# Kernel optimization log

Hardware: AMD Instinct MI355X
Metric: run time of the kernel (lower is better)

## Reference

```python
import jax, jax.numpy as jnp
import numpy as np

NEG_SLOPE = 0.2


def _gcn_conv(x, edge_index, W, b):
    # Standard GCNConv: y = D^-1/2 (A + I) D^-1/2 (x W) + b
    N = x.shape[0]
    loop = jnp.arange(N, dtype=edge_index.dtype)
    src = jnp.concatenate([edge_index[0], loop])  # [E+N]
    dst = jnp.concatenate([edge_index[1], loop])  # [E+N]
    deg = jax.ops.segment_sum(jnp.ones_like(dst, dtype=x.dtype), dst, num_segments=N)
    dinv = jnp.where(deg > 0, jax.lax.rsqrt(deg), 0.0)
    norm = dinv[src] * dinv[dst]                  # [E+N]
    h = x @ W                                     # [N, out] dense GEMM
    msg = h[src] * norm[:, None]                  # irregular gather, [E+N, out]
    agg = jax.ops.segment_sum(msg, dst, num_segments=N)  # irregular scatter
    return agg + b


def setup_inputs() -> dict:
    key = jax.random.key(0)
    ks = jax.random.split(key, 5)
    N, E, d_in, d_hid = 50000, 800000, 256, 512
    s = lambda fan_in, fan_out: np.sqrt(6.0 / (fan_in + fan_out))
    return {
        "x": jax.random.normal(ks[0], (N, d_in), dtype=jnp.float32),
        "edge_index": jax.random.randint(ks[1], (2, E), 0, N, dtype=jnp.int64),
        "W_gcn": jax.random.uniform(ks[2], (d_in, d_hid), jnp.float32, -s(d_in, d_hid), s(d_in, d_hid)),
        "b_gcn": jnp.zeros((d_hid,), jnp.float32),
        "W2": jax.random.uniform(ks[3], (d_hid, d_hid), jnp.float32, -s(d_hid, d_hid), s(d_hid, d_hid)),
        "b2": jnp.zeros((d_hid,), jnp.float32),
        "W_out": jax.random.uniform(ks[4], (d_hid, 1), jnp.float32, -s(d_hid, 1), s(d_hid, 1)),
        "b_out": jnp.zeros((1,), jnp.float32),
    }


def reference(x, edge_index, W_gcn, b_gcn, W2, b2, W_out, b_out):
    h = _gcn_conv(x, edge_index, W_gcn, b_gcn)           # [N, 512]
    h = jax.nn.leaky_relu(h, NEG_SLOPE)
    h = jax.nn.leaky_relu(h @ W2 + b2, NEG_SLOPE)        # [N, 512]
    return h @ W_out + b_out                             # [N, 1]
```

## Files before the change

### kernel.cpp

```cpp
#include <hip/hip_runtime.h>

#define D_IN  256
#define D_HID 512
#define NEG_SLOPE 0.2f
#define SCAN_CHUNK 2048

typedef __attribute__((ext_vector_type(8))) short short8;
typedef __attribute__((ext_vector_type(4))) float floatx4;

__device__ __forceinline__ unsigned short f2bf(float f) {
    unsigned int u = __float_as_uint(f);
    u += 0x7fffu + ((u >> 16) & 1u);
    return (unsigned short)(u >> 16);
}
__device__ __forceinline__ float bf2f(unsigned short u) {
    return __uint_as_float(((unsigned int)u) << 16);
}

__device__ __forceinline__ int eidx(const void* ei, long pos, int is64) {
    return is64 ? (int)((const long long*)ei)[pos] : ((const int*)ei)[pos];
}

__global__ __launch_bounds__(256) void k_init(int* __restrict__ deg, int N,
                                              const unsigned int* __restrict__ ei,
                                              int npairs, int* flag,
                                              const float* __restrict__ W_gcn,
                                              unsigned short* __restrict__ Wgt,
                                              const float* __restrict__ W2,
                                              unsigned short* __restrict__ W2t,
                                              const float* __restrict__ b_out,
                                              float* __restrict__ out) {
    int t = blockIdx.x * blockDim.x + threadIdx.x;
    if (blockIdx.x == 0) {
        __shared__ int nz;
        if (threadIdx.x == 0) nz = 0;
        __syncthreads();
        for (int p = threadIdx.x; p < npairs; p += blockDim.x)
            if (ei[2 * p + 1] != 0) nz = 1;
        __syncthreads();
        if (threadIdx.x == 0) *flag = nz ? 0 : 1;
    }
    if (t < D_IN * D_HID) {
        int n = t / D_IN, k = t - n * D_IN;
        Wgt[t] = f2bf(W_gcn[(long)k * D_HID + n]);
        return;
    }
    int u = t - D_IN * D_HID;
    if (u < D_HID * D_HID) {
        int n = u / D_HID, k = u - n * D_HID;
        W2t[u] = f2bf(W2[(long)k * D_HID + n]);
        return;
    }
    u -= D_HID * D_HID;
    if (u < N) { deg[u] = 0; out[u] = b_out[0]; }
}

__global__ void k_deg_count(const void* __restrict__ ei, const int* __restrict__ flag,
                            int* __restrict__ deg, int E) {
    int e = blockIdx.x * blockDim.x + threadIdx.x;
    if (e < E) atomicAdd(&deg[eidx(ei, (long)E + e, *flag)], 1);
}

__global__ __launch_bounds__(256) void k_scan1(const int* __restrict__ deg,
                                               int* __restrict__ bsum, int N) {
    int base = blockIdx.x * SCAN_CHUNK;
    int hi = min(base + SCAN_CHUNK, N);
    int s = 0;
    for (int i = base + threadIdx.x; i < hi; i += 256) s += deg[i];
#pragma unroll
    for (int off = 32; off > 0; off >>= 1) s += __shfl_down(s, off, 64);
    __shared__ int lds[4];
    if ((threadIdx.x & 63) == 0) lds[threadIdx.x >> 6] = s;
    __syncthreads();
    if (threadIdx.x == 0) bsum[blockIdx.x] = lds[0] + lds[1] + lds[2] + lds[3];
}

__global__ __launch_bounds__(256) void k_scan23(const int* __restrict__ deg,
                                                const int* __restrict__ bsum, int NB,
                                                int* __restrict__ offs,
                                                int* __restrict__ cursor,
                                                float* __restrict__ dinv, int N) {
    __shared__ int lds[256];
    int t = threadIdx.x;
    int bbase = 0;
    for (int i = 0; i < NB; ++i) bbase += (i < blockIdx.x) ? bsum[i] : 0;
    if (blockIdx.x == NB - 1 && t == 0) offs[N] = bbase + bsum[NB - 1];
    int base = blockIdx.x * SCAN_CHUNK;
    int lo = base + t * 8;
    int v[8], s = 0;
#pragma unroll
    for (int j = 0; j < 8; ++j) {
        int i = lo + j;
        v[j] = (i < N) ? deg[i] : 0;
        s += v[j];
    }
    lds[t] = s;
    __syncthreads();
    for (int d = 1; d < 256; d <<= 1) {
        int add = (t >= d) ? lds[t - d] : 0;
        __syncthreads();
        lds[t] += add;
        __syncthreads();
    }
    int run = bbase + ((t > 0) ? lds[t - 1] : 0);
#pragma unroll
    for (int j = 0; j < 8; ++j) {
        int i = lo + j;
        if (i < N) {
            offs[i] = run; cursor[i] = run;
            dinv[i] = rsqrtf(1.0f + (float)v[j]);
            run += v[j];
        }
    }
}

__global__ __launch_bounds__(256) void k_prescale(const float* __restrict__ x,
                                                  const float* __restrict__ dinv,
                                                  unsigned short* __restrict__ xb, int N) {
    long t = (long)blockIdx.x * blockDim.x + threadIdx.x;
    long total = (long)N * D_IN / 4;
    if (t >= total) return;
    int row = (int)(t >> 6);
    float s = dinv[row];
    float4 v = *(const float4*)(x + t * 4);
    ushort4 o;
    o.x = f2bf(v.x * s); o.y = f2bf(v.y * s); o.z = f2bf(v.z * s); o.w = f2bf(v.w * s);
    *(ushort4*)(xb + t * 4) = o;
}

__global__ void k_fill(const void* __restrict__ ei, const int* __restrict__ flag,
                       int* __restrict__ cursor, int* __restrict__ esrc, int E) {
    int e = blockIdx.x * blockDim.x + threadIdx.x;
    if (e >= E) return;
    int is64 = *flag;
    int s = eidx(ei, e, is64), d = eidx(ei, (long)E + e, is64);
    int pos = atomicAdd(&cursor[d], 1);
    esrc[pos] = s;
}

__global__ __launch_bounds__(256) void k_gather(const unsigned short* __restrict__ xb,
                                                const int* __restrict__ offs,
                                                const int* __restrict__ esrc,
                                                const float* __restrict__ dinv,
                                                unsigned short* __restrict__ aggb, int N) {
    int node = blockIdx.x * 4 + (threadIdx.x >> 6);
    if (node >= N) return;
    int lane = threadIdx.x & 63;
    int half = lane >> 5;
    int colofs = (lane & 31) * 8;
    float di = dinv[node];
    const unsigned short* xbc = xb + colofs;

    float a[8];
    {
        short8 v = *(const short8*)(xbc + (long)node * D_IN);
#pragma unroll
        for (int j = 0; j < 8; ++j)
            a[j] = (half == 0) ? bf2f((unsigned short)v[j]) : 0.f;
    }

    int beg = offs[node], end = offs[node + 1];
    int e = beg;
    for (; e + 16 <= end; e += 16) {
        int s0 = esrc[e      + half];
        int s1 = esrc[e +  2 + half];
        int s2 = esrc[e +  4 + half];
        int s3 = esrc[e +  6 + half];
        int s4 = esrc[e +  8 + half];
        int s5 = esrc[e + 10 + half];
        int s6 = esrc[e + 12 + half];
        int s7 = esrc[e + 14 + half];
        short8 u0 = *(const short8*)(xbc + (long)s0 * D_IN);
        short8 u1 = *(const short8*)(xbc + (long)s1 * D_IN);
        short8 u2 = *(const short8*)(xbc + (long)s2 * D_IN);
        short8 u3 = *(const short8*)(xbc + (long)s3 * D_IN);
        short8 u4 = *(const short8*)(xbc + (long)s4 * D_IN);
        short8 u5 = *(const short8*)(xbc + (long)s5 * D_IN);
        short8 u6 = *(const short8*)(xbc + (long)s6 * D_IN);
        short8 u7 = *(const short8*)(xbc + (long)s7 * D_IN);
#pragma unroll
        for (int j = 0; j < 8; ++j) {
            float t0 = bf2f((unsigned short)u0[j]) + bf2f((unsigned short)u1[j]);
            float t1 = bf2f((unsigned short)u2[j]) + bf2f((unsigned short)u3[j]);
            float t2 = bf2f((unsigned short)u4[j]) + bf2f((unsigned short)u5[j]);
            float t3 = bf2f((unsigned short)u6[j]) + bf2f((unsigned short)u7[j]);
            a[j] += (t0 + t1) + (t2 + t3);
        }
    }
    for (; e + 8 <= end; e += 8) {
        int s0 = esrc[e     + half];
        int s1 = esrc[e + 2 + half];
        int s2 = esrc[e + 4 + half];
        int s3 = esrc[e + 6 + half];
        short8 u0 = *(const short8*)(xbc + (long)s0 * D_IN);
        short8 u1 = *(const short8*)(xbc + (long)s1 * D_IN);
        short8 u2 = *(const short8*)(xbc + (long)s2 * D_IN);
        short8 u3 = *(const short8*)(xbc + (long)s3 * D_IN);
#pragma unroll
        for (int j = 0; j < 8; ++j) {
            float t0 = bf2f((unsigned short)u0[j]) + bf2f((unsigned short)u1[j]);
            float t1 = bf2f((unsigned short)u2[j]) + bf2f((unsigned short)u3[j]);
            a[j] += t0 + t1;
        }
    }
    for (; e < end; e += 2) {
        int j0 = e + half;
        int jj = (j0 < end) ? j0 : end - 1;
        int s = esrc[jj];
        float w = (j0 < end) ? 1.f : 0.f;
        short8 u = *(const short8*)(xbc + (long)s * D_IN);
#pragma unroll
        for (int j = 0; j < 8; ++j)
            a[j] += w * bf2f((unsigned short)u[j]);
    }

#pragma unroll
    for (int j = 0; j < 8; ++j) a[j] += __shfl_xor(a[j], 32, 64);

    if (half == 0) {
        short8 o;
#pragma unroll
        for (int j = 0; j < 8; ++j) o[j] = (short)f2bf(a[j] * di);
        *(short8*)(aggb + (long)node * D_IN + colofs) = o;
    }
}

__device__ __forceinline__ void async_cp16(const unsigned short* gp, unsigned short* lp) {
    __builtin_amdgcn_global_load_lds((const __attribute__((address_space(1))) void*)gp,
                                     (__attribute__((address_space(3))) void*)lp, 16, 0, 0);
}

__device__ __forceinline__ void stage_sw64(const unsigned short* src, int strideK,
                                           int rowMax, unsigned short* lds, int tid) {
#pragma unroll
    for (int rr = 0; rr < 4; ++rr) {
        int c = rr * 256 + tid;
        int row = c >> 3;
        int ci = (c & 7) ^ (row & 7);
        if (row > rowMax) row = rowMax;
        async_cp16(src + (long)row * strideK + ci * 8, lds + c * 8);
    }
}

__device__ __forceinline__ bool map_block(int b, int M, int& m0, int& n0) {
    int x = b & 7, slot = b >> 3;
    int mt = x + 8 * (slot >> 2);
    m0 = mt * 128; n0 = (slot & 3) * 128;
    return m0 < M;
}

__global__ __launch_bounds__(256) void k_gemm_bf16(const unsigned short* __restrict__ A,
                                                   const unsigned short* __restrict__ Bt,
                                                   const float* __restrict__ bias,
                                                   unsigned short* __restrict__ C,
                                                   int M, int K) {
    __shared__ __align__(16) unsigned short As[128 * 64];
    __shared__ __align__(16) unsigned short Bs[128 * 64];
    __shared__ __align__(16) unsigned short Ep[32 * 128];
    const int tid  = threadIdx.x;
    const int lane = tid & 63, wave = tid >> 6;
    int m0, n0;
    if (!map_block(blockIdx.x, M, m0, n0)) return;
    const int r = lane & 15, q = lane >> 4;
    const int xv = r & 7;
    const int wm = (wave & 1) * 64, wn = (wave >> 1) * 64;
    const int band = wm >> 6;

    floatx4 acc[4][4];
#pragma unroll
    for (int i = 0; i < 4; ++i)
#pragma unroll
        for (int j = 0; j < 4; ++j) acc[i][j] = (floatx4){0.f, 0.f, 0.f, 0.f};

    for (int k0 = 0; k0 < K; k0 += 64) {
        stage_sw64(A + (long)m0 * K + k0, K, M - 1 - m0, As, tid);
        stage_sw64(Bt + (long)n0 * K + k0, K, 127, Bs, tid);
        __syncthreads();

#pragma unroll
        for (int s = 0; s < 2; ++s) {
            int slotbase = s * 4 + q;
            short8 af[4], bf[4];
#pragma unroll
            for (int i = 0; i < 4; ++i)
                af[i] = *(const short8*)(As + (wm + i * 16 + r) * 64 + (slotbase ^ xv) * 8);
#pragma unroll
            for (int j = 0; j < 4; ++j)
                bf[j] = *(const short8*)(Bs + (wn + j * 16 + r) * 64 + (slotbase ^ xv) * 8);
#pragma unroll
            for (int i = 0; i < 4; ++i)
#pragma unroll
                for (int j = 0; j < 4; ++j)
                    acc[i][j] = __builtin_amdgcn_mfma_f32_16x16x32_bf16(af[i], bf[j], acc[i][j], 0, 0, 0);
        }
        __syncthreads();
    }

    float bv[4];
#pragma unroll
    for (int j = 0; j < 4; ++j) bv[j] = bias[n0 + wn + j * 16 + r];

#pragma unroll
    for (int i = 0; i < 4; ++i) {
#pragma unroll
        for (int j = 0; j < 4; ++j) {
#pragma unroll
            for (int t2 = 0; t2 < 4; ++t2) {
                float v = acc[i][j][t2] + bv[j];
                v = v > 0.f ? v : NEG_SLOPE * v;
                Ep[(band * 16 + q * 4 + t2) * 128 + wn + j * 16 + r] = f2bf(v);
            }
        }
        __syncthreads();
#pragma unroll
        for (int rr = 0; rr < 2; ++rr) {
            int c = rr * 256 + tid;
            int lrow = c >> 4, ccol = c & 15;
            int grow = m0 + (lrow >> 4) * 64 + i * 16 + (lrow & 15);
            if (grow < M) {
                short8 v = *(const short8*)(Ep + lrow * 128 + ccol * 8);
                *(short8*)(C + (long)grow * D_HID + n0 + ccol * 8) = v;
            }
        }
        __syncthreads();
    }
}

__global__ __launch_bounds__(256) void k_gemm2f(const unsigned short* __restrict__ A,
                                                const unsigned short* __restrict__ Bt,
                                                const float* __restrict__ bias,
                                                const float* __restrict__ wout,
                                                float* __restrict__ out,
                                                int M, int K) {
    __shared__ __align__(16) unsigned short As[128 * 64];
    __shared__ __align__(16) unsigned short Bs[128 * 64];
    const int tid  = threadIdx.x;
    const int lane = tid & 63, wave = tid >> 6;
    int m0, n0;
    if (!map_block(blockIdx.x, M, m0, n0)) return;
    const int r = lane & 15, q = lane >> 4;
    const int xv = r & 7;
    const int wm = (wave & 1) * 64, wn = (wave >> 1) * 64;

    floatx4 acc[4][4];
#pragma unroll
    for (int i = 0; i < 4; ++i)
#pragma unroll
        for (int j = 0; j < 4; ++j) acc[i][j] = (floatx4){0.f, 0.f, 0.f, 0.f};

    for (int k0 = 0; k0 < K; k0 += 64) {
        stage_sw64(A + (long)m0 * K + k0, K, M - 1 - m0, As, tid);
        stage_sw64(Bt + (long)n0 * K + k0, K, 127, Bs, tid);
        __syncthreads();

#pragma unroll
        for (int s = 0; s < 2; ++s) {
            int slotbase = s * 4 + q;
            short8 af[4], bf[4];
#pragma unroll
            for (int i = 0; i < 4; ++i)
                af[i] = *(const short8*)(As + (wm + i * 16 + r) * 64 + (slotbase ^ xv) * 8);
#pragma unroll
            for (int j = 0; j < 4; ++j)
                bf[j] = *(const short8*)(Bs + (wn + j * 16 + r) * 64 + (slotbase ^ xv) * 8);
#pragma unroll
            for (int i = 0; i < 4; ++i)
#pragma unroll
                for (int j = 0; j < 4; ++j)
                    acc[i][j] = __builtin_amdgcn_mfma_f32_16x16x32_bf16(af[i], bf[j], acc[i][j], 0, 0, 0);
        }
        __syncthreads();
    }

    float bv[4], wv[4];
#pragma unroll
    for (int j = 0; j < 4; ++j) {
        int col = n0 + wn + j * 16 + r;
        bv[j] = bias[col];
        wv[j] = wout[col];
    }
#pragma unroll
    for (int i = 0; i < 4; ++i) {
#pragma unroll
        for (int t2 = 0; t2 < 4; ++t2) {
            float p = 0.f;
#pragma unroll
            for (int j = 0; j < 4; ++j) {
                float v = acc[i][j][t2] + bv[j];
                v = v > 0.f ? v : NEG_SLOPE * v;
                p += v * wv[j];
            }
            p += __shfl_xor(p, 8, 64);
            p += __shfl_xor(p, 4, 64);
            p += __shfl_xor(p, 2, 64);
            p += __shfl_xor(p, 1, 64);
            if (r == 0) {
                int row = m0 + wm + i * 16 + q * 4 + t2;
                if (row < M) atomicAdd(&out[row], p);
            }
        }
    }
}

extern "C" void kernel_launch(void* const* d_in, const int* in_sizes, int n_in,
                              void* d_out, int out_size, void* d_ws, size_t ws_size,
                              hipStream_t stream) {
    const float* x     = (const float*)d_in[0];
    const void*  ei    = d_in[1];
    const float* W_gcn = (const float*)d_in[2];
    const float* b_gcn = (const float*)d_in[3];
    const float* W2    = (const float*)d_in[4];
    const float* b2    = (const float*)d_in[5];
    const float* W_out = (const float*)d_in[6];
    const float* b_out = (const float*)d_in[7];
    float* out = (float*)d_out;

    const int N = in_sizes[0] / D_IN;
    const int E = in_sizes[1] / 2;
    const int NB = (N + SCAN_CHUNK - 1) / SCAN_CHUNK;

    char* w = (char*)d_ws;
    size_t off = 0;
    auto alloc = [&](size_t bytes) { char* p = w + off; off = (off + bytes + 255) & ~(size_t)255; return p; };
    int*            flag   = (int*)alloc(256);
    float*          dinv   = (float*)alloc((size_t)N * 4);
    int*            deg_i  = (int*)alloc((size_t)N * 4);
    int*            offs   = (int*)alloc((size_t)(N + 1) * 4);
    int*            cursor = (int*)alloc((size_t)N * 4);
    int*            bsum   = (int*)alloc((size_t)NB * 4);
    int*            esrc   = (int*)alloc((size_t)(E + 16) * 4);
    unsigned short* xb     = (unsigned short*)alloc((size_t)N * D_IN * 2);
    unsigned short* aggb   = (unsigned short*)alloc((size_t)N * D_IN * 2);
    unsigned short* h1     = (unsigned short*)alloc((size_t)N * D_HID * 2);
    unsigned short* Wgt    = (unsigned short*)alloc((size_t)D_IN * D_HID * 2);
    unsigned short* W2t    = (unsigned short*)alloc((size_t)D_HID * D_HID * 2);

    int npairs = E < 2048 ? E : 2048;
    long init_threads = (long)D_IN * D_HID + (long)D_HID * D_HID + N;
    k_init<<<(unsigned)((init_threads + 255) / 256), 256, 0, stream>>>(
        deg_i, N, (const unsigned int*)ei, npairs, flag,
        W_gcn, Wgt, W2, W2t, b_out, out);

    k_deg_count<<<(E + 255) / 256, 256, 0, stream>>>(ei, flag, deg_i, E);
    k_scan1<<<NB, 256, 0, stream>>>(deg_i, bsum, N);
    k_scan23<<<NB, 256, 0, stream>>>(deg_i, bsum, NB, offs, cursor, dinv, N);

    long pthreads = (long)N * D_IN / 4;
    k_prescale<<<(unsigned)((pthreads + 255) / 256), 256, 0, stream>>>(x, dinv, xb, N);
    k_fill<<<(E + 255) / 256, 256, 0, stream>>>(ei, flag, cursor, esrc, E);

    k_gather<<<(N + 3) / 4, 256, 0, stream>>>(xb, offs, esrc, dinv, aggb, N);

    int mtiles = (N + 127) / 128;
    int gblocks = ((mtiles + 7) / 8) * 8 * 4;
    k_gemm_bf16<<<gblocks, 256, 0, stream>>>(aggb, Wgt, b_gcn, h1, N, D_IN);
    k_gemm2f<<<gblocks, 256, 0, stream>>>(h1, W2t, b2, W_out, out, N, D_HID);
}
```

Before: 336.7 us.

## Persistent-wave gather over node ranges and tiled LDS weight transpose kernel

The gather kernel now launches a fixed grid of 2048 blocks, and each wave handles a contiguous range of nodes. While processing one node it prefetches the next node's offset, dinv and self row, and the 16-edge unrolled path is dropped. Weight transposition moves out of k_init into a separate kernel that transposes 64x64 tiles through LDS, so both global reads and writes are coalesced instead of strided. The cost is one extra launch, and the gather may lose latency hiding from fewer waves and less unrolling.

```diff
diff --git a/kernel.cpp b/kernel.cpp
--- a/kernel.cpp
+++ b/kernel.cpp
@@ -4,6 +4,7 @@
 #define D_HID 512
 #define NEG_SLOPE 0.2f
 #define SCAN_CHUNK 2048
+#define GATHER_BLOCKS 2048
 
 typedef __attribute__((ext_vector_type(8))) short short8;
 typedef __attribute__((ext_vector_type(4))) float floatx4;
@@ -24,10 +25,6 @@
 __global__ __launch_bounds__(256) void k_init(int* __restrict__ deg, int N,
                                               const unsigned int* __restrict__ ei,
                                               int npairs, int* flag,
-                                              const float* __restrict__ W_gcn,
-                                              unsigned short* __restrict__ Wgt,
-                                              const float* __restrict__ W2,
-                                              unsigned short* __restrict__ W2t,
                                               const float* __restrict__ b_out,
                                               float* __restrict__ out) {
     int t = blockIdx.x * blockDim.x + threadIdx.x;
@@ -40,19 +37,32 @@
         __syncthreads();
         if (threadIdx.x == 0) *flag = nz ? 0 : 1;
     }
-    if (t < D_IN * D_HID) {
-        int n = t / D_IN, k = t - n * D_IN;
-        Wgt[t] = f2bf(W_gcn[(long)k * D_HID + n]);
-        return;
-    }
-    int u = t - D_IN * D_HID;
-    if (u < D_HID * D_HID) {
-        int n = u / D_HID, k = u - n * D_HID;
-        W2t[u] = f2bf(W2[(long)k * D_HID + n]);
-        return;
-    }
-    u -= D_HID * D_HID;
-    if (u < N) { deg[u] = 0; out[u] = b_out[0]; }
+    if (t < N) { deg[t] = 0; out[t] = b_out[0]; }
+}
+
+__global__ __launch_bounds__(256) void k_wtrans(const float* __restrict__ Wa,
+                                                unsigned short* __restrict__ Wat,
+                                                const float* __restrict__ Wb,
+                                                unsigned short* __restrict__ Wbt) {
+    __shared__ float t[64][65];
+    int b = blockIdx.x;
+    const float* W; unsigned short* Wt; int K, Nc, tk, tn;
+    if (b < 32) { W = Wa; Wt = Wat; K = 256; Nc = 512; tk = b & 3; tn = b >> 2; }
+    else { b -= 32; W = Wb; Wt = Wbt; K = 512; Nc = 512; tk = b & 7; tn = b >> 3; }
+    int k0 = tk * 64, n0 = tn * 64;
+    int c = threadIdx.x & 63;
+    int r0 = threadIdx.x >> 6;
+#pragma unroll
+    for (int i = 0; i < 16; ++i) {
+        int r = r0 + i * 4;
+        t[r][c] = W[(long)(k0 + r) * Nc + n0 + c];
+    }
+    __syncthreads();
+#pragma unroll
+    for (int i = 0; i < 16; ++i) {
+        int r = r0 + i * 4;
+        Wt[(long)(n0 + r) * K + k0 + c] = f2bf(t[c][r]);
+    }
 }
 
 __global__ void k_deg_count(const void* __restrict__ ei, const int* __restrict__ flag,
@@ -142,86 +152,78 @@
                                                 const int* __restrict__ offs,
                                                 const int* __restrict__ esrc,
                                                 const float* __restrict__ dinv,
-                                                unsigned short* __restrict__ aggb, int N) {
-    int node = blockIdx.x * 4 + (threadIdx.x >> 6);
-    if (node >= N) return;
+                                                unsigned short* __restrict__ aggb,
+                                                int N, int nwaves) {
+    int wid = blockIdx.x * 4 + (threadIdx.x >> 6);
+    int lo = (int)((long)wid * N / nwaves);
+    int hi = (int)((long)(wid + 1) * N / nwaves);
+    if (lo >= hi) return;
     int lane = threadIdx.x & 63;
     int half = lane >> 5;
     int colofs = (lane & 31) * 8;
+    const unsigned short* xbc = xb + colofs;
+
+    int node = lo;
+    int bg = offs[node];
+    int en = offs[node + 1];
     float di = dinv[node];
-    const unsigned short* xbc = xb + colofs;
-
-    float a[8];
-    {
-        short8 v = *(const short8*)(xbc + (long)node * D_IN);
+    short8 sv = *(const short8*)(xbc + (long)node * D_IN);
+
+    while (true) {
+        int nxt = node + 1;
+        bool has = nxt < hi;
+        int en2 = 0; float di2 = 0.f; short8 sv2;
+        if (has) {
+            en2 = offs[nxt + 1];
+            di2 = dinv[nxt];
+            sv2 = *(const short8*)(xbc + (long)nxt * D_IN);
+        }
+
+        float a[8];
 #pragma unroll
         for (int j = 0; j < 8; ++j)
-            a[j] = (half == 0) ? bf2f((unsigned short)v[j]) : 0.f;
-    }
-
-    int beg = offs[node], end = offs[node + 1];
-    int e = beg;
-    for (; e + 16 <= end; e += 16) {
-        int s0 = esrc[e      + half];
-        int s1 = esrc[e +  2 + half];
-        int s2 = esrc[e +  4 + half];
-        int s3 = esrc[e +  6 + half];
-        int s4 = esrc[e +  8 + half];
-        int s5 = esrc[e + 10 + half];
-        int s6 = esrc[e + 12 + half];
-        int s7 = esrc[e + 14 + half];
-        short8 u0 = *(const short8*)(xbc + (long)s0 * D_IN);
-        short8 u1 = *(const short8*)(xbc + (long)s1 * D_IN);
-        short8 u2 = *(const short8*)(xbc + (long)s2 * D_IN);
-        short8 u3 = *(const short8*)(xbc + (long)s3 * D_IN);
-        short8 u4 = *(const short8*)(xbc + (long)s4 * D_IN);
-        short8 u5 = *(const short8*)(xbc + (long)s5 * D_IN);
-        short8 u6 = *(const short8*)(xbc + (long)s6 * D_IN);
-        short8 u7 = *(const short8*)(xbc + (long)s7 * D_IN);
-#pragma unroll
-        for (int j = 0; j < 8; ++j) {
-            float t0 = bf2f((unsigned short)u0[j]) + bf2f((unsigned short)u1[j]);
-            float t1 = bf2f((unsigned short)u2[j]) + bf2f((unsigned short)u3[j]);
-            float t2 = bf2f((unsigned short)u4[j]) + bf2f((unsigned short)u5[j]);
-            float t3 = bf2f((unsigned short)u6[j]) + bf2f((unsigned short)u7[j]);
-            a[j] += (t0 + t1) + (t2 + t3);
-        }
-    }
-    for (; e + 8 <= end; e += 8) {
-        int s0 = esrc[e     + half];
-        int s1 = esrc[e + 2 + half];
-        int s2 = esrc[e + 4 + half];
-        int s3 = esrc[e + 6 + half];
-        short8 u0 = *(const short8*)(xbc + (long)s0 * D_IN);
-        short8 u1 = *(const short8*)(xbc + (long)s1 * D_IN);
-        short8 u2 = *(const short8*)(xbc + (long)s2 * D_IN);
-        short8 u3 = *(const short8*)(xbc + (long)s3 * D_IN);
-#pragma unroll
-        for (int j = 0; j < 8; ++j) {
-            float t0 = bf2f((unsigned short)u0[j]) + bf2f((unsigned short)u1[j]);
-            float t1 = bf2f((unsigned short)u2[j]) + bf2f((unsigned short)u3[j]);
-            a[j] += t0 + t1;
-        }
-    }
-    for (; e < end; e += 2) {
-        int j0 = e + half;
-        int jj = (j0 < end) ? j0 : end - 1;
-        int s = esrc[jj];
-        float w = (j0 < end) ? 1.f : 0.f;
-        short8 u = *(const short8*)(xbc + (long)s * D_IN);
-#pragma unroll
-        for (int j = 0; j < 8; ++j)
-            a[j] += w * bf2f((unsigned short)u[j]);
-    }
-
-#pragma unroll
-    for (int j = 0; j < 8; ++j) a[j] += __shfl_xor(a[j], 32, 64);
-
-    if (half == 0) {
-        short8 o;
-#pragma unroll
-        for (int j = 0; j < 8; ++j) o[j] = (short)f2bf(a[j] * di);
-        *(short8*)(aggb + (long)node * D_IN + colofs) = o;
+            a[j] = (half == 0) ? bf2f((unsigned short)sv[j]) : 0.f;
+
+        int e = bg;
+        for (; e + 8 <= en; e += 8) {
+            int s0 = esrc[e + half];
+            int s1 = esrc[e + 2 + half];
+            int s2 = esrc[e + 4 + half];
+            int s3 = esrc[e + 6 + half];
+            short8 u0 = *(const short8*)(xbc + (long)s0 * D_IN);
+            short8 u1 = *(const short8*)(xbc + (long)s1 * D_IN);
+            short8 u2 = *(const short8*)(xbc + (long)s2 * D_IN);
+            short8 u3 = *(const short8*)(xbc + (long)s3 * D_IN);
+#pragma unroll
+            for (int j = 0; j < 8; ++j) {
+                float t0 = bf2f((unsigned short)u0[j]) + bf2f((unsigned short)u1[j]);
+                float t1 = bf2f((unsigned short)u2[j]) + bf2f((unsigned short)u3[j]);
+                a[j] += t0 + t1;
+            }
+        }
+        for (; e < en; e += 2) {
+            int j0 = e + half;
+            int jj = (j0 < en) ? j0 : en - 1;
+            int s = esrc[jj];
+            float w = (j0 < en) ? 1.f : 0.f;
+            short8 u = *(const short8*)(xbc + (long)s * D_IN);
+#pragma unroll
+            for (int j = 0; j < 8; ++j)
+                a[j] += w * bf2f((unsigned short)u[j]);
+        }
+
+#pragma unroll
+        for (int j = 0; j < 8; ++j) a[j] += __shfl_xor(a[j], 32, 64);
+
+        if (half == 0) {
+            short8 o;
+#pragma unroll
+            for (int j = 0; j < 8; ++j) o[j] = (short)f2bf(a[j] * di);
+            *(short8*)(aggb + (long)node * D_IN + colofs) = o;
+        }
+
+        if (!has) break;
+        node = nxt; bg = en; en = en2; di = di2; sv = sv2;
     }
 }
 
@@ -436,10 +438,9 @@
     unsigned short* W2t    = (unsigned short*)alloc((size_t)D_HID * D_HID * 2);
 
     int npairs = E < 2048 ? E : 2048;
-    long init_threads = (long)D_IN * D_HID + (long)D_HID * D_HID + N;
-    k_init<<<(unsigned)((init_threads + 255) / 256), 256, 0, stream>>>(
-        deg_i, N, (const unsigned int*)ei, npairs, flag,
-        W_gcn, Wgt, W2, W2t, b_out, out);
+    k_init<<<(N + 255) / 256, 256, 0, stream>>>(deg_i, N, (const unsigned int*)ei,
+                                                npairs, flag, b_out, out);
+    k_wtrans<<<96, 256, 0, stream>>>(W_gcn, Wgt, W2, W2t);
 
     k_deg_count<<<(E + 255) / 256, 256, 0, stream>>>(ei, flag, deg_i, E);
     k_scan1<<<NB, 256, 0, stream>>>(deg_i, bsum, N);
@@ -449,7 +450,9 @@
     k_prescale<<<(unsigned)((pthreads + 255) / 256), 256, 0, stream>>>(x, dinv, xb, N);
     k_fill<<<(E + 255) / 256, 256, 0, stream>>>(ei, flag, cursor, esrc, E);
 
-    k_gather<<<(N + 3) / 4, 256, 0, stream>>>(xb, offs, esrc, dinv, aggb, N);
+    int gblocks_gather = GATHER_BLOCKS;
+    int nwaves = gblocks_gather * 4;
+    k_gather<<<gblocks_gather, 256, 0, stream>>>(xb, offs, esrc, dinv, aggb, N, nwaves);
 
     int mtiles = (N + 127) / 128;
     int gblocks = ((mtiles + 7) / 8) * 8 * 4;
```

Result: no change. 338.3 us (+0.5%).
